# Performance work log

Measured on AMD Instinct MI355X. Metric: run time of the kernel, lower is better.

Reference implementation:

```python
import jax, jax.numpy as jnp
import numpy as np

N_PIX = 65536   # 256x256 render
N_GAUSS = 2048
N_COL = 3


def setup_inputs() -> dict:
    key = jax.random.key(0)
    k1, k2, k3, k4 = jax.random.split(key, 4)
    x = jax.random.uniform(k1, (N_PIX, 2), dtype=jnp.float32)           # pixel coords
    mus = jax.random.uniform(k2, (N_GAUSS, 2), dtype=jnp.float32)       # Gaussian means
    # SPD covariances: A A^T + sigma*I  (small spatial extent ~0.05)
    A = jax.random.normal(k3, (N_GAUSS, 2, 2), dtype=jnp.float32) * 0.05
    covs = jnp.einsum('mij,mkj->mik', A, A) + 0.01 * jnp.eye(2, dtype=jnp.float32)
    cols = jax.random.uniform(k4, (N_GAUSS, N_COL), dtype=jnp.float32)  # RGB per Gaussian
    return {"x": x, "mus": mus, "covs": covs, "cols": cols}


def reference(x, mus, covs, cols):
    # d: [N, M, 2] pixel-to-mean offsets
    d = x[:, None, :] - mus[None, :, :]
    # solve(covs, d) per (pixel, Gaussian) == cov_inv @ d; covs depend only on Gaussian,
    # so invert once per Gaussian (same math as torch.linalg.solve per pair).
    cov_inv = jnp.linalg.inv(covs)                      # [M, 2, 2]
    maha = jnp.einsum('nmi,mij,nmj->nm', d, cov_inv, d)  # [N, M] Mahalanobis distances
    w = jnp.exp(-0.5 * maha)                             # [N, M] Gaussian weights
    # weighted sum of colors over Gaussians: [N, M] @ [M, 3] -> [N, 3]
    return jnp.einsum('nm,mc->nc', w, cols)
```

## Files before the change

### kernel.cpp

```cpp
#include <hip/hip_runtime.h>

#define N_PIX   65536
#define N_GAUSS 2048
#define GCHUNK  256
#define NCHUNK  (N_GAUSS / GCHUNK)
#define NPIXBLK (N_PIX / 256)

__global__ __launch_bounds__(256, 8) void render_kernel(
        const float2* __restrict__ x,
        const float* __restrict__ mus,
        const float* __restrict__ covs,
        const float* __restrict__ cols,
        float* __restrict__ out) {
    __shared__ float4 lg[2 * GCHUNK];

    int pixblk = blockIdx.x % NPIXBLK;
    int chunk  = blockIdx.x / NPIXBLK;
    int t = threadIdx.x;

    {
        int m = chunk * GCHUNK + t;
        float c00 = covs[4*m+0], c01 = covs[4*m+1];
        float c10 = covs[4*m+2], c11 = covs[4*m+3];
        float inv_det = 1.0f / (c00*c11 - c01*c10);
        const float k = -0.7213475204444817f;
        float ia =  c11 * inv_det;
        float ib = -c01 * inv_det;
        float ic =  c00 * inv_det;
        lg[2*t+0] = make_float4(mus[2*m+0], mus[2*m+1], k*ia, k*2.0f*ib);
        lg[2*t+1] = make_float4(k*ic, cols[3*m+0], cols[3*m+1], cols[3*m+2]);
    }
    __syncthreads();

    int n = pixblk * 256 + t;
    float2 p = x[n];
    float accr = 0.f, accg = 0.f, accb = 0.f;
    #pragma unroll 8
    for (int m = 0; m < GCHUNK; ++m) {
        float4 g0 = lg[2*m+0];
        float4 g1 = lg[2*m+1];
        float dx = p.x - g0.x;
        float dy = p.y - g0.y;
        float t1 = fmaf(g0.z, dx, g0.w * dy);
        float q  = fmaf(t1, dx, g1.x * (dy*dy));
        float w  = __builtin_amdgcn_exp2f(q);
        accr = fmaf(w, g1.y, accr);
        accg = fmaf(w, g1.z, accg);
        accb = fmaf(w, g1.w, accb);
    }
    unsafeAtomicAdd(&out[3*n+0], accr);
    unsafeAtomicAdd(&out[3*n+1], accg);
    unsafeAtomicAdd(&out[3*n+2], accb);
}

extern "C" void kernel_launch(void* const* d_in, const int* in_sizes, int n_in,
                              void* d_out, int out_size, void* d_ws, size_t ws_size,
                              hipStream_t stream) {
    const float* x    = (const float*)d_in[0];
    const float* mus  = (const float*)d_in[1];
    const float* covs = (const float*)d_in[2];
    const float* cols = (const float*)d_in[3];
    float* out = (float*)d_out;

    hipMemsetAsync(out, 0, (size_t)out_size * sizeof(float), stream);

    render_kernel<<<NPIXBLK * NCHUNK, 256, 0, stream>>>(
        (const float2*)x, mus, covs, cols, out);
}
```

Measured before the change: 101.3 us.

## Precompute expanded quadratic coefficients per Gaussian and read them via uniform loads

```diff
diff --git a/kernel.cpp b/kernel.cpp
--- a/kernel.cpp
+++ b/kernel.cpp
@@ -5,48 +5,63 @@
 #define GCHUNK  256
 #define NCHUNK  (N_GAUSS / GCHUNK)
 #define NPIXBLK (N_PIX / 256)
+#define GSTRIDE 16
+
+__global__ __launch_bounds__(256) void prep_kernel(
+        const float* __restrict__ mus,
+        const float* __restrict__ covs,
+        const float* __restrict__ cols,
+        float* __restrict__ gc) {
+    int m = blockIdx.x * blockDim.x + threadIdx.x;
+    if (m >= N_GAUSS) return;
+    float c00 = covs[4*m+0], c01 = covs[4*m+1];
+    float c10 = covs[4*m+2], c11 = covs[4*m+3];
+    float inv_det = 1.0f / (c00*c11 - c01*c10);
+    float ia =  c11 * inv_det;
+    float ib = -c01 * inv_det;
+    float ic =  c00 * inv_det;
+    float mx = mus[2*m+0], my = mus[2*m+1];
+    const float k = -0.7213475204444817f;
+    float A = k * ia;
+    float B = k * 2.0f * ib;
+    float C = k * ic;
+    float D = -2.0f * k * (ia*mx + ib*my);
+    float E = -2.0f * k * (ib*mx + ic*my);
+    float F = k * (ia*mx*mx + 2.0f*ib*mx*my + ic*my*my);
+    float* r = gc + m * GSTRIDE;
+    r[0] = A; r[1] = B; r[2] = C; r[3] = D; r[4] = E; r[5] = F;
+    r[6] = cols[3*m+0]; r[7] = cols[3*m+1]; r[8] = cols[3*m+2];
+    r[9] = 0.f; r[10] = 0.f; r[11] = 0.f; r[12] = 0.f; r[13] = 0.f; r[14] = 0.f; r[15] = 0.f;
+}
 
 __global__ __launch_bounds__(256, 8) void render_kernel(
         const float2* __restrict__ x,
-        const float* __restrict__ mus,
-        const float* __restrict__ covs,
-        const float* __restrict__ cols,
+        const float* __restrict__ gc,
         float* __restrict__ out) {
-    __shared__ float4 lg[2 * GCHUNK];
-
     int pixblk = blockIdx.x % NPIXBLK;
     int chunk  = blockIdx.x / NPIXBLK;
     int t = threadIdx.x;
 
-    {
-        int m = chunk * GCHUNK + t;
-        float c00 = covs[4*m+0], c01 = covs[4*m+1];
-        float c10 = covs[4*m+2], c11 = covs[4*m+3];
-        float inv_det = 1.0f / (c00*c11 - c01*c10);
-        const float k = -0.7213475204444817f;
-        float ia =  c11 * inv_det;
-        float ib = -c01 * inv_det;
-        float ic =  c00 * inv_det;
-        lg[2*t+0] = make_float4(mus[2*m+0], mus[2*m+1], k*ia, k*2.0f*ib);
-        lg[2*t+1] = make_float4(k*ic, cols[3*m+0], cols[3*m+1], cols[3*m+2]);
-    }
-    __syncthreads();
-
     int n = pixblk * 256 + t;
     float2 p = x[n];
+    float px2  = p.x * p.x;
+    float py2  = p.y * p.y;
+    float pxpy = p.x * p.y;
     float accr = 0.f, accg = 0.f, accb = 0.f;
+
+    const float* g = gc + (size_t)chunk * GCHUNK * GSTRIDE;
     #pragma unroll 8
     for (int m = 0; m < GCHUNK; ++m) {
-        float4 g0 = lg[2*m+0];
-        float4 g1 = lg[2*m+1];
-        float dx = p.x - g0.x;
-        float dy = p.y - g0.y;
-        float t1 = fmaf(g0.z, dx, g0.w * dy);
-        float q  = fmaf(t1, dx, g1.x * (dy*dy));
-        float w  = __builtin_amdgcn_exp2f(q);
-        accr = fmaf(w, g1.y, accr);
-        accg = fmaf(w, g1.z, accg);
-        accb = fmaf(w, g1.w, accb);
+        const float* c = g + m * GSTRIDE;
+        float q = fmaf(c[0], px2,
+                  fmaf(c[1], pxpy,
+                  fmaf(c[2], py2,
+                  fmaf(c[3], p.x,
+                  fmaf(c[4], p.y, c[5])))));
+        float w = __builtin_amdgcn_exp2f(q);
+        accr = fmaf(w, c[6], accr);
+        accg = fmaf(w, c[7], accg);
+        accb = fmaf(w, c[8], accb);
     }
     unsafeAtomicAdd(&out[3*n+0], accr);
     unsafeAtomicAdd(&out[3*n+1], accg);
@@ -61,9 +76,10 @@
     const float* covs = (const float*)d_in[2];
     const float* cols = (const float*)d_in[3];
     float* out = (float*)d_out;
+    float* gc  = (float*)d_ws;
 
     hipMemsetAsync(out, 0, (size_t)out_size * sizeof(float), stream);
 
-    render_kernel<<<NPIXBLK * NCHUNK, 256, 0, stream>>>(
-        (const float2*)x, mus, covs, cols, out);
+    prep_kernel<<<(N_GAUSS + 255) / 256, 256, 0, stream>>>(mus, covs, cols, gc);
+    render_kernel<<<NPIXBLK * NCHUNK, 256, 0, stream>>>((const float2*)x, gc, out);
 }
```

Result: slower. 114.1 us (+12.6%).
